# Kernel tuning notes

Hardware: AMD Instinct MI355X
Metric: run time of the kernel (lower is better)

Reference implementation:

```python
import jax, jax.numpy as jnp
import numpy as np

N_GRAPHS = 32
NUM_NODES = 2848
N = N_GRAPHS * NUM_NODES  # 91136
E = 1_000_000
K = 3   # num_stacks
T = 5   # num_layers
HID = 32
EPS = 1e-5


def setup_inputs() -> dict:
    key = jax.random.key(0)
    ks = jax.random.split(key, 32)
    s = 0.1
    rn = lambda k, shp: (jax.random.normal(k, shp, jnp.float32) * s)
    inp = {
        "x": jax.random.normal(ks[0], (N, 2), jnp.float32),
        "edge_index": jax.random.randint(ks[1], (2, E), 0, N, dtype=jnp.int32).astype(jnp.int64),
        "weights": jax.random.uniform(ks[2], (E,), jnp.float32),
        "batch": (jnp.arange(N) // NUM_NODES).astype(jnp.int64),
        # ARMAConv1: 2 -> 32
        "iw1": rn(ks[3], (K, 2, HID)),
        "w1": rn(ks[4], (T - 1, K, HID, HID)),
        "rw1": rn(ks[5], (T, K, 2, HID)),
        "b1": rn(ks[6], (T, K, 1, HID)),
        "g1": jnp.ones((HID,), jnp.float32), "be1": jnp.zeros((HID,), jnp.float32),
        # ARMAConv2: 32 -> 32
        "iw2": rn(ks[7], (K, HID, HID)),
        "w2": rn(ks[8], (T - 1, K, HID, HID)),
        "rw2": rn(ks[9], (T, K, HID, HID)),
        "b2": rn(ks[10], (T, K, 1, HID)),
        "g2": jnp.ones((HID,), jnp.float32), "be2": jnp.zeros((HID,), jnp.float32),
        # ARMAConv3: 32 -> 1
        "iw3": rn(ks[11], (K, HID, 1)),
        "w3": rn(ks[12], (T - 1, K, 1, 1)),
        "rw3": rn(ks[13], (T, K, HID, 1)),
        "b3": rn(ks[14], (T, K, 1, 1)),
        "g3": jnp.ones((1,), jnp.float32), "be3": jnp.zeros((1,), jnp.float32),
        # classifier Linear(1, 1)
        "cw": rn(ks[15], (1, 1)),
        "cb": jnp.zeros((1,), jnp.float32),
    }
    return inp


def gcn_norm(row, col, w, n):
    # deg over targets, sym normalization, no self loops (PyG ARMAConv default)
    deg = jnp.zeros((n,), w.dtype).at[col].add(w)
    dis = jnp.where(deg > 0, jax.lax.rsqrt(jnp.where(deg > 0, deg, 1.0)), 0.0)
    return dis[row] * w * dis[col]


def arma_conv(x, row, col, norm, iw, w, rw, b):
    # x: [N, Fin]; returns [N, Fout] (mean over K stacks)
    out = None
    for t in range(T):
        if t == 0:
            h = jnp.einsum('nf,kfo->kno', x, iw)          # [K, N, Fout]
        else:
            h = jnp.einsum('kno,kop->knp', out, w[t - 1])
        msg = h[:, row, :] * norm[None, :, None]           # [K, E, Fout]
        agg = jnp.zeros_like(h).at[:, col, :].add(msg)     # scatter to targets
        out = jax.nn.relu(agg + jnp.einsum('nf,kfo->kno', x, rw[t]) + b[t])
    return out.mean(axis=0)


def batch_norm(x, g, b):
    m = x.mean(axis=0)
    v = x.var(axis=0)  # biased, as torch BatchNorm1d (training stats)
    return (x - m) * jax.lax.rsqrt(v + EPS) * g + b


def reference(x, edge_index, weights, batch,
              iw1, w1, rw1, b1, g1, be1,
              iw2, w2, rw2, b2, g2, be2,
              iw3, w3, rw3, b3, g3, be3,
              cw, cb):
    row, col = edge_index[0], edge_index[1]
    norm = gcn_norm(row, col, weights, N)

    h = arma_conv(x, row, col, norm, iw1, w1, rw1, b1)
    h = jax.nn.relu(batch_norm(h, g1, be1))
    h = arma_conv(h, row, col, norm, iw2, w2, rw2, b2)
    h = jax.nn.relu(batch_norm(h, g2, be2))
    h = arma_conv(h, row, col, norm, iw3, w3, rw3, b3)
    h = jax.nn.relu(batch_norm(h, g3, be3))  # [N, 1]

    # to_dense_batch: each graph has exactly NUM_NODES nodes -> reshape
    xd = h.reshape(N_GRAPHS, NUM_NODES, 1)
    logits_nodes = (xd @ cw.T + cb).squeeze(-1)   # [B, NUM_NODES]
    logits_graph = logits_nodes.max(axis=1)       # [B]
    return logits_nodes, logits_graph
```

## Files before the change

kernel.cpp:

```cpp
#include <hip/hip_runtime.h>
#include <hip/hip_fp16.h>

#define N_GRAPHS 32
#define NUM_NODES 2848
#define NTOT (N_GRAPHS * NUM_NODES)
#define NE 1000000
#define KS 3
#define TL 5
#define HID 32
#define EPSV 1e-5f
#define SCAN_B 256
#define NBLK (NTOT / SCAN_B)
#define NBINS 64
#define CNTN (NBINS * NBLK)
#define CNTB (CNTN / SCAN_B)
#define NT8 (NTOT * 8)
#define NB128 (NTOT / 128)
#define SRCMASK 0x1FFFFu

typedef unsigned uintx4 __attribute__((ext_vector_type(4)));


__device__ __forceinline__ float2 unpk(unsigned u) {
    return make_float2(__uint_as_float(u << 16), __uint_as_float(u & 0xffff0000u));
}
__device__ __forceinline__ unsigned bf16rn(float f) {
    unsigned x = __float_as_uint(f);
    return (x + 0x7fffu + ((x >> 16) & 1u)) >> 16;
}
__device__ __forceinline__ unsigned pk(float a, float b) {
    return bf16rn(a) | (bf16rn(b) << 16);
}
__device__ __forceinline__ float dec_nm(unsigned q) {
    return __half2float(__ushort_as_half((unsigned short)(q >> 17)));
}


__global__ void k_cnt(const int* __restrict__ col, int* __restrict__ indegS) {
    int e = blockIdx.x * blockDim.x + threadIdx.x;
    if (e < NE) atomicAdd(&indegS[(col[e] << 2) | (e & 3)], 1);
}

__global__ void k_merge(const int* __restrict__ indegS, int* __restrict__ indeg) {
    int n = blockIdx.x * blockDim.x + threadIdx.x;
    if (n < NTOT) {
        int4 v = ((const int4*)indegS)[n];
        indeg[n] = v.x + v.y + v.z + v.w;
    }
}

__global__ void k_lhist(const int* __restrict__ indeg, int* __restrict__ cnt) {
    __shared__ int h[NBINS];
    int t = threadIdx.x;
    if (t < NBINS) h[t] = 0;
    __syncthreads();
    int n = blockIdx.x * SCAN_B + t;
    atomicAdd(&h[min(indeg[n], NBINS - 1)], 1);
    __syncthreads();
    if (t < NBINS) cnt[t * NBLK + blockIdx.x] = h[t];
}

__global__ void k_scan1(const int* __restrict__ in, int* __restrict__ bsum) {
    __shared__ int s[SCAN_B];
    int i = blockIdx.x * SCAN_B + threadIdx.x;
    s[threadIdx.x] = in[i];
    __syncthreads();
    for (int st = SCAN_B / 2; st >= 1; st >>= 1) {
        if (threadIdx.x < st) s[threadIdx.x] += s[threadIdx.x + st];
        __syncthreads();
    }
    if (threadIdx.x == 0) bsum[blockIdx.x] = s[0];
}

__global__ void k_scan2(int* __restrict__ bsum, int n) {
    __shared__ int s[512];
    int t = threadIdx.x;
    int v = (t < n) ? bsum[t] : 0;
    s[t] = v;
    __syncthreads();
    for (int off = 1; off < 512; off <<= 1) {
        int a = (t >= off) ? s[t - off] : 0;
        __syncthreads();
        s[t] += a;
        __syncthreads();
    }
    if (t < n) bsum[t] = s[t] - v;
}

__global__ void k_scan3(const int* __restrict__ in, const int* __restrict__ bsum,
                        int* __restrict__ out, int sentIdx, int sentVal) {
    __shared__ int s[SCAN_B];
    int i = blockIdx.x * SCAN_B + threadIdx.x;
    int v = in[i];
    s[threadIdx.x] = v;
    __syncthreads();
    for (int off = 1; off < SCAN_B; off <<= 1) {
        int a = (threadIdx.x >= off) ? s[threadIdx.x - off] : 0;
        __syncthreads();
        s[threadIdx.x] += a;
        __syncthreads();
    }
    out[i] = bsum[blockIdx.x] + s[threadIdx.x] - v;
    if (i == 0 && sentIdx >= 0) out[sentIdx] = sentVal;
}

__global__ void k_rank(const int* __restrict__ indeg, const int* __restrict__ cnt,
                       int* __restrict__ perm, int* __restrict__ invperm,
                       int* __restrict__ indegp) {
    __shared__ int base[NBINS];
    __shared__ int cur[NBINS];
    int t = threadIdx.x;
    if (t < NBINS) { base[t] = cnt[t * NBLK + blockIdx.x]; cur[t] = 0; }
    __syncthreads();
    int n = blockIdx.x * SCAN_B + t;
    int dg = indeg[n];
    int b = min(dg, NBINS - 1);
    int pos = base[b] + atomicAdd(&cur[b], 1);
    perm[pos] = n;
    invperm[n] = pos;
    indegp[pos] = dg;
}

__global__ void k_xp(const float2* __restrict__ x, const int* __restrict__ perm,
                     float2* __restrict__ xp) {
    int i = blockIdx.x * blockDim.x + threadIdx.x;
    if (i < NTOT) xp[i] = x[perm[i]];
}

__global__ void k_fill(const int* __restrict__ row, const int* __restrict__ col,
                       const float* __restrict__ w, const int* __restrict__ invperm,
                       int* __restrict__ cursor, unsigned* __restrict__ adjc) {
    int e = blockIdx.x * blockDim.x + threadIdx.x;
    if (e < NE) {
        int pr = invperm[row[e]], pc = invperm[col[e]];
        int p = atomicAdd(&cursor[pc], 1);
        unsigned short hb = __half_as_ushort(__float2half(w[e]));
        adjc[p] = ((unsigned)hb << 17) | (unsigned)pr;
    }
}

__global__ void k_degdis(const unsigned* __restrict__ adjc, const int* __restrict__ offs,
                         float* __restrict__ disp) {
    int n = blockIdx.x * blockDim.x + threadIdx.x;
    if (n >= NTOT) return;
    int e0 = offs[n], e1 = offs[n + 1];
    float d = 0.f;
    for (int e = e0; e < e1; ++e) d += dec_nm(adjc[e]);
    disp[n] = (d > 0.f) ? rsqrtf(d) : 0.f;
}

__global__ void k_norm(unsigned* __restrict__ adjc, const int* __restrict__ offs,
                       const float* __restrict__ disp) {
    int n = blockIdx.x * blockDim.x + threadIdx.x;
    if (n >= NTOT) return;
    float dc = disp[n];
    int e0 = offs[n], e1 = offs[n + 1];
    for (int e = e0; e < e1; ++e) {
        unsigned q = adjc[e];
        float nm = dc * dec_nm(q) * disp[q & SRCMASK];
        unsigned short hb = __half_as_ushort(__float2half(nm));
        adjc[e] = ((unsigned)hb << 17) | (q & SRCMASK);
    }
}


__global__ __launch_bounds__(256) void k_gath(
    const unsigned* __restrict__ SRC, const int* __restrict__ offs,
    const unsigned* __restrict__ adjc, unsigned* __restrict__ P) {
    int tid = threadIdx.x;
    int u = tid & 1;
    int nl = tid >> 1;
    int bid = blockIdx.x;
    int s = bid / NB128;
    int node = (bid - s * NB128) * 128 + nl;
    const uintx4* src = (const uintx4*)(SRC + (size_t)s * NT8);
    float a0 = 0.f, a1 = 0.f, a2 = 0.f, a3 = 0.f, a4 = 0.f, a5 = 0.f, a6 = 0.f, a7 = 0.f;
    int e0 = offs[node], e1 = offs[node + 1];
    int e = e0;
    for (; e + 4 <= e1; e += 4) {
        unsigned q0 = __builtin_nontemporal_load(adjc + e);
        unsigned q1 = __builtin_nontemporal_load(adjc + e + 1);
        unsigned q2 = __builtin_nontemporal_load(adjc + e + 2);
        unsigned q3 = __builtin_nontemporal_load(adjc + e + 3);
        uintx4 v0 = src[(q0 & SRCMASK) * 2 + u];
        uintx4 v1 = src[(q1 & SRCMASK) * 2 + u];
        uintx4 v2 = src[(q2 & SRCMASK) * 2 + u];
        uintx4 v3 = src[(q3 & SRCMASK) * 2 + u];
        float n0 = dec_nm(q0), n1 = dec_nm(q1), n2 = dec_nm(q2), n3 = dec_nm(q3);
        float2 t;
        t = unpk(v0.x); a0 += n0 * t.x; a1 += n0 * t.y;
        t = unpk(v0.y); a2 += n0 * t.x; a3 += n0 * t.y;
        t = unpk(v0.z); a4 += n0 * t.x; a5 += n0 * t.y;
        t = unpk(v0.w); a6 += n0 * t.x; a7 += n0 * t.y;
        t = unpk(v1.x); a0 += n1 * t.x; a1 += n1 * t.y;
        t = unpk(v1.y); a2 += n1 * t.x; a3 += n1 * t.y;
        t = unpk(v1.z); a4 += n1 * t.x; a5 += n1 * t.y;
        t = unpk(v1.w); a6 += n1 * t.x; a7 += n1 * t.y;
        t = unpk(v2.x); a0 += n2 * t.x; a1 += n2 * t.y;
        t = unpk(v2.y); a2 += n2 * t.x; a3 += n2 * t.y;
        t = unpk(v2.z); a4 += n2 * t.x; a5 += n2 * t.y;
        t = unpk(v2.w); a6 += n2 * t.x; a7 += n2 * t.y;
        t = unpk(v3.x); a0 += n3 * t.x; a1 += n3 * t.y;
        t = unpk(v3.y); a2 += n3 * t.x; a3 += n3 * t.y;
        t = unpk(v3.z); a4 += n3 * t.x; a5 += n3 * t.y;
        t = unpk(v3.w); a6 += n3 * t.x; a7 += n3 * t.y;
    }
    for (; e < e1; ++e) {
        unsigned q0 = __builtin_nontemporal_load(adjc + e);
        uintx4 v0 = src[(q0 & SRCMASK) * 2 + u];
        float n0 = dec_nm(q0);
        float2 t;
        t = unpk(v0.x); a0 += n0 * t.x; a1 += n0 * t.y;
        t = unpk(v0.y); a2 += n0 * t.x; a3 += n0 * t.y;
        t = unpk(v0.z); a4 += n0 * t.x; a5 += n0 * t.y;
        t = unpk(v0.w); a6 += n0 * t.x; a7 += n0 * t.y;
    }
    uintx4 o;
    o.x = pk(a0, a1); o.y = pk(a2, a3); o.z = pk(a4, a5); o.w = pk(a6, a7);
    __builtin_nontemporal_store(o, (uintx4*)(P + (size_t)s * NT8 + (size_t)node * 8) + u);
}


template<int FIN, bool PERK, bool LAST>
__global__ __launch_bounds__(256) void k_xform(
    const unsigned* __restrict__ P, const float* __restrict__ xin,
    const float* __restrict__ W, const float* __restrict__ rw,
    const float* __restrict__ bb, unsigned* __restrict__ OUTn,
    float* __restrict__ xm, float* __restrict__ stats) {
    constexpr int NSEC = PERK ? 6 : 2;
    constexpr int ND = 128;
    __shared__ unsigned sp[KS][ND][17];
    __shared__ float xr[FIN == 32 ? ND : 1][FIN == 32 ? 33 : 1];
    int tid = threadIdx.x;
    int node0 = blockIdx.x * ND;
    for (int t4 = tid; t4 < NSEC * 256; t4 += 256) {
        int s = t4 >> 8, r = t4 & 255, n = r >> 1, u4 = (r & 1) * 4;
        uintx4 v = *(const uintx4*)(P + (size_t)s * NT8 + (size_t)(node0 + n) * 8 + u4);
        int kk = PERK ? (s >> 1) : 0;
        int base = (s & 1) * 8 + u4;
        sp[kk][n][base]     = v.x;
        sp[kk][n][base + 1] = v.y;
        sp[kk][n][base + 2] = v.z;
        sp[kk][n][base + 3] = v.w;
    }
    if constexpr (FIN == 32) {
        for (int t4 = tid; t4 < ND * 8; t4 += 256) {
            int n = t4 >> 3, j4 = (t4 & 7) * 4;
            float4 v = ((const float4*)xin)[(size_t)(node0 + n) * 8 + (t4 & 7)];
            xr[n][j4] = v.x; xr[n][j4 + 1] = v.y; xr[n][j4 + 2] = v.z; xr[n][j4 + 3] = v.w;
        }
    }
    __syncthreads();
    int f2 = tid & 15, nl = tid >> 4;
    int nbase = nl * 8;
    float2 xv2[8];
    if constexpr (FIN == 2) {
#pragma unroll
        for (int n = 0; n < 8; ++n) xv2[n] = ((const float2*)xin)[node0 + nbase + n];
    }
    float m0[8] = {}, m1[8] = {};
    unsigned uo[KS][8];
#pragma unroll
    for (int k = 0; k < KS; ++k) {
        const int kk = PERK ? k : 0;
        float2 bv = ((const float2*)(bb + k * HID))[f2];
        float h0[8], h1[8];
#pragma unroll
        for (int n = 0; n < 8; ++n) { h0[n] = bv.x; h1[n] = bv.y; }
        const float2* W2 = (const float2*)(W + (size_t)k * HID * HID);
        const float2* R2 = (const float2*)(rw + (size_t)k * FIN * HID);
#pragma unroll 4
        for (int i2 = 0; i2 < 16; ++i2) {
            float2 wf0 = W2[(2 * i2) * 16 + f2];
            float2 wf1 = W2[(2 * i2 + 1) * 16 + f2];
            float2 rf0, rf1;
            if constexpr (FIN == 32) {
                rf0 = R2[(2 * i2) * 16 + f2];
                rf1 = R2[(2 * i2 + 1) * 16 + f2];
            }
#pragma unroll
            for (int n = 0; n < 8; ++n) {
                float2 sv = unpk(sp[kk][nbase + n][i2]);
                h0[n] += sv.x * wf0.x + sv.y * wf1.x;
                h1[n] += sv.x * wf0.y + sv.y * wf1.y;
                if constexpr (FIN == 32) {
                    float x0 = xr[nbase + n][2 * i2], x1 = xr[nbase + n][2 * i2 + 1];
                    h0[n] += x0 * rf0.x + x1 * rf1.x;
                    h1[n] += x0 * rf0.y + x1 * rf1.y;
                }
            }
        }
        if constexpr (FIN == 2) {
            float2 r0 = R2[0 * 16 + f2], r1 = R2[1 * 16 + f2];
#pragma unroll
            for (int n = 0; n < 8; ++n) {
                h0[n] += xv2[n].x * r0.x + xv2[n].y * r1.x;
                h1[n] += xv2[n].x * r0.y + xv2[n].y * r1.y;
            }
        }
#pragma unroll
        for (int n = 0; n < 8; ++n) {
            h0[n] = fmaxf(h0[n], 0.f);
            h1[n] = fmaxf(h1[n], 0.f);
            if constexpr (LAST) {
                m0[n] += h0[n]; m1[n] += h1[n];
            } else {
                uo[k][n] = pk(h0[n], h1[n]);
            }
        }
    }
    if constexpr (LAST) {
        float sv0 = 0.f, sq0 = 0.f, sv1 = 0.f, sq1 = 0.f;
#pragma unroll
        for (int n = 0; n < 8; ++n) {
            float v0 = m0[n] * (1.f / 3.f), v1 = m1[n] * (1.f / 3.f);
            ((float2*)xm)[(size_t)(node0 + nbase + n) * 16 + f2] = make_float2(v0, v1);
            sv0 += v0; sq0 += v0 * v0;
            sv1 += v1; sq1 += v1 * v1;
        }
        float* red = (float*)sp;
        __syncthreads();
        red[0 * 256 + f2 * 16 + nl] = sv0;
        red[1 * 256 + f2 * 16 + nl] = sq0;
        red[2 * 256 + f2 * 16 + nl] = sv1;
        red[3 * 256 + f2 * 16 + nl] = sq1;
        __syncthreads();
        if (nl == 0) {
            float a = 0.f, b = 0.f, c = 0.f, d = 0.f;
#pragma unroll
            for (int j = 0; j < 16; ++j) {
                a += red[0 * 256 + f2 * 16 + j];
                b += red[1 * 256 + f2 * 16 + j];
                c += red[2 * 256 + f2 * 16 + j];
                d += red[3 * 256 + f2 * 16 + j];
            }
            atomicAdd(&stats[2 * f2], a);
            atomicAdd(&stats[HID + 2 * f2], b);
            atomicAdd(&stats[2 * f2 + 1], c);
            atomicAdd(&stats[HID + 2 * f2 + 1], d);
        }
    } else {
#pragma unroll
        for (int k = 0; k < KS; ++k)
#pragma unroll
            for (int n = 0; n < 8; ++n)
                sp[k][nbase + n][f2] = uo[k][n];
        __syncthreads();
        for (int t4 = tid; t4 < 6 * 256; t4 += 256) {
            int s = t4 >> 8, r = t4 & 255, n = r >> 1, u4 = (r & 1) * 4;
            int kk = s >> 1;
            int base = (s & 1) * 8 + u4;
            uintx4 v;
            v.x = sp[kk][n][base];
            v.y = sp[kk][n][base + 1];
            v.z = sp[kk][n][base + 2];
            v.w = sp[kk][n][base + 3];
            __builtin_nontemporal_store(
                v, (uintx4*)(OUTn + (size_t)s * NT8 + (size_t)(node0 + n) * 8 + u4));
        }
    }
}


__global__ void k_gath2(const float2* __restrict__ xp, const int* __restrict__ offs,
                        const unsigned* __restrict__ adjc, float2* __restrict__ pag) {
    int node = blockIdx.x * blockDim.x + threadIdx.x;
    if (node >= NTOT) return;
    float a0 = 0.f, a1 = 0.f;
    int e0 = offs[node], e1 = offs[node + 1];
    int e = e0;
    for (; e + 4 <= e1; e += 4) {
        unsigned q0 = __builtin_nontemporal_load(adjc + e);
        unsigned q1 = __builtin_nontemporal_load(adjc + e + 1);
        unsigned q2 = __builtin_nontemporal_load(adjc + e + 2);
        unsigned q3 = __builtin_nontemporal_load(adjc + e + 3);
        float2 x0 = xp[q0 & SRCMASK], x1 = xp[q1 & SRCMASK];
        float2 x2 = xp[q2 & SRCMASK], x3 = xp[q3 & SRCMASK];
        float n0 = dec_nm(q0), n1 = dec_nm(q1), n2 = dec_nm(q2), n3 = dec_nm(q3);
        a0 += n0 * x0.x + n1 * x1.x + n2 * x2.x + n3 * x3.x;
        a1 += n0 * x0.y + n1 * x1.y + n2 * x2.y + n3 * x3.y;
    }
    for (; e < e1; ++e) {
        unsigned q0 = __builtin_nontemporal_load(adjc + e);
        float2 xs = xp[q0 & SRCMASK];
        float nm = dec_nm(q0);
        a0 += nm * xs.x; a1 += nm * xs.y;
    }
    pag[node] = make_float2(a0, a1);
}

__global__ void k_x0(const float2* __restrict__ pag, const float2* __restrict__ xp,
                     const float* __restrict__ iw, const float* __restrict__ rw0,
                     const float* __restrict__ b0, unsigned* __restrict__ OUT) {
    int tid = blockIdx.x * blockDim.x + threadIdx.x;
    int f2 = tid & 15;
    int node = tid >> 4;
    float2 pv = pag[node];
    float2 xn = xp[node];
#pragma unroll
    for (int k = 0; k < KS; ++k) {
        const float2* iw2 = (const float2*)(iw + k * 2 * HID);
        const float2* rw2 = (const float2*)(rw0 + k * 2 * HID);
        float2 wi0 = iw2[0 * 16 + f2], wi1 = iw2[1 * 16 + f2];
        float2 wr0 = rw2[0 * 16 + f2], wr1 = rw2[1 * 16 + f2];
        float2 bv = ((const float2*)(b0 + k * HID))[f2];
        float o0 = fmaxf(pv.x * wi0.x + pv.y * wi1.x + xn.x * wr0.x + xn.y * wr1.x + bv.x, 0.f);
        float o1 = fmaxf(pv.x * wi0.y + pv.y * wi1.y + xn.x * wr0.y + xn.y * wr1.y + bv.y, 0.f);
        OUT[(size_t)(k * 2 + (f2 >> 3)) * NT8 + (size_t)node * 8 + (f2 & 7)] = pk(o0, o1);
    }
}


__global__ void k_rec3(const float* __restrict__ xb, const float* __restrict__ iw3,
                       const float* __restrict__ rw3, const float* __restrict__ b3,
                       float4* __restrict__ H0, float4* __restrict__ RT) {
    int n = blockIdx.x * blockDim.x + threadIdx.x;
    if (n >= NTOT) return;
    float xr[HID];
#pragma unroll
    for (int j = 0; j < 8; ++j) {
        float4 v = ((const float4*)xb)[(size_t)n * 8 + j];
        xr[4 * j] = v.x; xr[4 * j + 1] = v.y; xr[4 * j + 2] = v.z; xr[4 * j + 3] = v.w;
    }
    {
        float a0 = 0.f, a1 = 0.f, a2 = 0.f;
#pragma unroll
        for (int i = 0; i < HID; ++i) {
            a0 += xr[i] * iw3[0 * HID + i];
            a1 += xr[i] * iw3[1 * HID + i];
            a2 += xr[i] * iw3[2 * HID + i];
        }
        H0[n] = make_float4(a0, a1, a2, 0.f);
    }
#pragma unroll
    for (int t = 0; t < TL; ++t) {
        float a0 = b3[t * KS + 0], a1 = b3[t * KS + 1], a2 = b3[t * KS + 2];
        const float* r = rw3 + (size_t)t * KS * HID;
#pragma unroll
        for (int i = 0; i < HID; ++i) {
            a0 += xr[i] * r[0 * HID + i];
            a1 += xr[i] * r[1 * HID + i];
            a2 += xr[i] * r[2 * HID + i];
        }
        RT[(size_t)t * NTOT + n] = make_float4(a0, a1, a2, 0.f);
    }
}

template<bool LAST>
__global__ void k_prop1(const float4* __restrict__ H, const float4* __restrict__ RT,
                        const float* __restrict__ W_t, const int* __restrict__ offs,
                        const unsigned* __restrict__ adjc, const int* __restrict__ perm,
                        float* __restrict__ outp) {
    int node = blockIdx.x * blockDim.x + threadIdx.x;
    if (node >= NTOT) return;
    float4 rt = RT[node];
    float a0 = rt.x, a1 = rt.y, a2 = rt.z;
    int e0 = offs[node], e1 = offs[node + 1];
    int e = e0;
    for (; e + 4 <= e1; e += 4) {
        unsigned q0 = __builtin_nontemporal_load(adjc + e);
        unsigned q1 = __builtin_nontemporal_load(adjc + e + 1);
        unsigned q2 = __builtin_nontemporal_load(adjc + e + 2);
        unsigned q3 = __builtin_nontemporal_load(adjc + e + 3);
        float4 h0 = H[q0 & SRCMASK], h1 = H[q1 & SRCMASK];
        float4 h2 = H[q2 & SRCMASK], h3 = H[q3 & SRCMASK];
        float n0 = dec_nm(q0), n1 = dec_nm(q1), n2 = dec_nm(q2), n3 = dec_nm(q3);
        a0 += n0 * h0.x; a1 += n0 * h0.y; a2 += n0 * h0.z;
        a0 += n1 * h1.x; a1 += n1 * h1.y; a2 += n1 * h1.z;
        a0 += n2 * h2.x; a1 += n2 * h2.y; a2 += n2 * h2.z;
        a0 += n3 * h3.x; a1 += n3 * h3.y; a2 += n3 * h3.z;
    }
    for (; e < e1; ++e) {
        unsigned q0 = __builtin_nontemporal_load(adjc + e);
        float4 h = H[q0 & SRCMASK];
        float nm = dec_nm(q0);
        a0 += nm * h.x; a1 += nm * h.y; a2 += nm * h.z;
    }
    a0 = fmaxf(a0, 0.f); a1 = fmaxf(a1, 0.f); a2 = fmaxf(a2, 0.f);
    if constexpr (LAST) {
        outp[perm[node]] = (a0 + a1 + a2) * (1.f / 3.f);
    } else {
        ((float4*)outp)[node] = make_float4(a0 * W_t[0], a1 * W_t[1], a2 * W_t[2], 0.f);
    }
}


__global__ void k_bnstats(const float* __restrict__ x, float* __restrict__ stats, int F) {
    __shared__ float s1[256];
    __shared__ float s2[256];
    int tid = threadIdx.x;
    int gid = blockIdx.x * blockDim.x + tid;
    int stride = gridDim.x * blockDim.x;
    int total = NTOT * F;
    float a = 0.f, b = 0.f;
    for (int i = gid; i < total; i += stride) {
        float v = x[i];
        a += v;
        b += v * v;
    }
    s1[tid] = a; s2[tid] = b;
    __syncthreads();
    for (int s = 128; s >= F; s >>= 1) {
        if (tid < s) { s1[tid] += s1[tid + s]; s2[tid] += s2[tid + s]; }
        __syncthreads();
    }
    if (tid < F) {
        atomicAdd(&stats[tid], s1[tid]);
        atomicAdd(&stats[F + tid], s2[tid]);
    }
}

__global__ void k_bnapply32(float* __restrict__ x, const float* __restrict__ stats,
                            const float* __restrict__ g, const float* __restrict__ be,
                            unsigned* __restrict__ xbf) {
    int tid = blockIdx.x * blockDim.x + threadIdx.x;
    int f2 = tid & 15;
    int node = tid >> 4;
    int f0 = 2 * f2, f1 = f0 + 1;
    float mm0 = stats[f0] * (1.f / NTOT);
    float vv0 = stats[HID + f0] * (1.f / NTOT) - mm0 * mm0;
    float mm1 = stats[f1] * (1.f / NTOT);
    float vv1 = stats[HID + f1] * (1.f / NTOT) - mm1 * mm1;
    float y0 = fmaxf((x[(size_t)node * 32 + f0] - mm0) * rsqrtf(vv0 + EPSV) * g[f0] + be[f0], 0.f);
    float y1 = fmaxf((x[(size_t)node * 32 + f1] - mm1) * rsqrtf(vv1 + EPSV) * g[f1] + be[f1], 0.f);
    x[(size_t)node * 32 + f0] = y0;
    x[(size_t)node * 32 + f1] = y1;
    if (xbf) xbf[(size_t)(f2 >> 3) * NT8 + (size_t)node * 8 + (f2 & 7)] = pk(y0, y1);
}

__global__ void k_bnapply1(float* __restrict__ x, const float* __restrict__ stats,
                           const float* __restrict__ g, const float* __restrict__ be) {
    int i = blockIdx.x * blockDim.x + threadIdx.x;
    if (i >= NTOT) return;
    float m = stats[0] * (1.f / NTOT);
    float v = stats[1] * (1.f / NTOT) - m * m;
    float y = (x[i] - m) * rsqrtf(v + EPSV) * g[0] + be[0];
    x[i] = fmaxf(y, 0.f);
}


__global__ void k_final(const float* __restrict__ h, const float* __restrict__ cw,
                        const float* __restrict__ cb, float* __restrict__ out) {
    __shared__ float smax[256];
    int g = blockIdx.x;
    float cwv = cw[0], cbv = cb[0];
    float mx = -INFINITY;
    for (int i = threadIdx.x; i < NUM_NODES; i += blockDim.x) {
        int nidx = g * NUM_NODES + i;
        float v = h[nidx] * cwv + cbv;
        out[nidx] = v;
        mx = fmaxf(mx, v);
    }
    smax[threadIdx.x] = mx;
    __syncthreads();
    for (int s = 128; s >= 1; s >>= 1) {
        if (threadIdx.x < s) smax[threadIdx.x] = fmaxf(smax[threadIdx.x], smax[threadIdx.x + s]);
        __syncthreads();
    }
    if (threadIdx.x == 0) out[NTOT + g] = smax[0];
}


extern "C" void kernel_launch(void* const* d_in, const int* in_sizes, int n_in,
                              void* d_out, int out_size, void* d_ws, size_t ws_size,
                              hipStream_t stream) {
    const float* x   = (const float*)d_in[0];
    const int*   ei  = (const int*)d_in[1];
    const int*   row = ei;
    const int*   col = ei + NE;
    const float* wts = (const float*)d_in[2];
    const float* iw1 = (const float*)d_in[4];
    const float* w1  = (const float*)d_in[5];
    const float* rw1 = (const float*)d_in[6];
    const float* b1  = (const float*)d_in[7];
    const float* g1  = (const float*)d_in[8];
    const float* be1 = (const float*)d_in[9];
    const float* iw2 = (const float*)d_in[10];
    const float* w2  = (const float*)d_in[11];
    const float* rw2 = (const float*)d_in[12];
    const float* b2  = (const float*)d_in[13];
    const float* g2  = (const float*)d_in[14];
    const float* be2 = (const float*)d_in[15];
    const float* iw3 = (const float*)d_in[16];
    const float* w3  = (const float*)d_in[17];
    const float* rw3 = (const float*)d_in[18];
    const float* b3  = (const float*)d_in[19];
    const float* g3  = (const float*)d_in[20];
    const float* be3 = (const float*)d_in[21];
    const float* cw  = (const float*)d_in[22];
    const float* cb  = (const float*)d_in[23];
    float* out = (float*)d_out;

    char* p = (char*)d_ws;
    auto alloc = [&](size_t bytes) {
        char* r = p;
        p += (bytes + 255) & ~(size_t)255;
        return r;
    };
    int*      indegS = (int*)alloc((size_t)NTOT * 16);
    int*      cnt    = (int*)alloc((size_t)CNTN * 4);
    float*    stats  = (float*)alloc(3 * 2 * HID * 4);
    char*     zend   = p;
    int*      indeg  = (int*)alloc((size_t)NTOT * 4);
    int*      bsum   = (int*)alloc((size_t)NBLK * 4);
    int*      offs   = (int*)alloc((size_t)(NTOT + 1) * 4);
    int*      cursor = (int*)alloc((size_t)NTOT * 4);
    int*      perm   = (int*)alloc((size_t)NTOT * 4);
    int*      invperm= (int*)alloc((size_t)NTOT * 4);
    int*      indegp = (int*)alloc((size_t)NTOT * 4);
    float*    disp   = (float*)alloc((size_t)NTOT * 4);
    unsigned* adjc   = (unsigned*)alloc((size_t)NE * 4);
    unsigned* OUTA   = (unsigned*)alloc((size_t)6 * NT8 * 4);
    unsigned* OUTB   = (unsigned*)alloc((size_t)6 * NT8 * 4);
    unsigned* P      = (unsigned*)alloc((size_t)6 * NT8 * 4);
    unsigned* xplane = (unsigned*)alloc((size_t)2 * NT8 * 4);
    float2*   xp     = (float2*)alloc((size_t)NTOT * 8);
    float2*   pag    = (float2*)alloc((size_t)NTOT * 8);
    float*    xa     = (float*)alloc((size_t)NTOT * HID * 4);
    float*    xb     = (float*)alloc((size_t)NTOT * HID * 4);
    float*    xc     = (float*)alloc((size_t)NTOT * 4);
    float4*   RT     = (float4*)alloc((size_t)TL * NTOT * 16);
    if ((size_t)(p - (char*)d_ws) > ws_size) return;

    const int tb = 256;
    const int ebl = (NE + tb - 1) / tb;
    const int nbl = NTOT / tb;
    const int g16 = NTOT * 16 / tb;

    hipMemsetAsync(indegS, 0, (size_t)(zend - (char*)indegS), stream);

    k_cnt<<<ebl, tb, 0, stream>>>(col, indegS);
    k_merge<<<nbl, tb, 0, stream>>>(indegS, indeg);
    k_lhist<<<NBLK, SCAN_B, 0, stream>>>(indeg, cnt);
    k_scan1<<<CNTB, SCAN_B, 0, stream>>>(cnt, bsum);
    k_scan2<<<1, 512, 0, stream>>>(bsum, CNTB);
    k_scan3<<<CNTB, SCAN_B, 0, stream>>>(cnt, bsum, cnt, -1, 0);
    k_rank<<<NBLK, SCAN_B, 0, stream>>>(indeg, cnt, perm, invperm, indegp);
    k_xp<<<nbl, tb, 0, stream>>>((const float2*)x, perm, xp);
    k_scan1<<<NBLK, SCAN_B, 0, stream>>>(indegp, bsum);
    k_scan2<<<1, 512, 0, stream>>>(bsum, NBLK);
    k_scan3<<<NBLK, SCAN_B, 0, stream>>>(indegp, bsum, offs, NTOT, NE);
    hipMemcpyAsync(cursor, offs, (size_t)NTOT * 4, hipMemcpyDeviceToDevice, stream);
    k_fill<<<ebl, tb, 0, stream>>>(row, col, wts, invperm, cursor, adjc);
    k_degdis<<<nbl, tb, 0, stream>>>(adjc, offs, disp);
    k_norm<<<nbl, tb, 0, stream>>>(adjc, offs, disp);

    {
        k_gath2<<<nbl, tb, 0, stream>>>(xp, offs, adjc, pag);
        k_x0<<<g16, tb, 0, stream>>>(pag, xp, iw1, rw1, b1, OUTA);
        unsigned* Hc = OUTA; unsigned* Hn = OUTB;
        for (int t = 1; t < TL - 1; ++t) {
            k_gath<<<6 * NB128, tb, 0, stream>>>(Hc, offs, adjc, P);
            k_xform<2, true, false><<<NB128, tb, 0, stream>>>(
                P, (const float*)xp, w1 + (size_t)(t - 1) * KS * HID * HID,
                rw1 + (size_t)t * KS * 2 * HID, b1 + (size_t)t * KS * HID, Hn,
                nullptr, nullptr);
            unsigned* tmp = Hc; Hc = Hn; Hn = tmp;
        }
        k_gath<<<6 * NB128, tb, 0, stream>>>(Hc, offs, adjc, P);
        k_xform<2, true, true><<<NB128, tb, 0, stream>>>(
            P, (const float*)xp, w1 + (size_t)(TL - 2) * KS * HID * HID,
            rw1 + (size_t)(TL - 1) * KS * 2 * HID, b1 + (size_t)(TL - 1) * KS * HID,
            nullptr, xa, stats);
        k_bnapply32<<<g16, tb, 0, stream>>>(xa, stats, g1, be1, xplane);
    }
    {
        k_gath<<<2 * NB128, tb, 0, stream>>>(xplane, offs, adjc, P);
        k_xform<32, false, false><<<NB128, tb, 0, stream>>>(
            P, xa, iw2, rw2, b2, OUTA, nullptr, nullptr);
        unsigned* Hc = OUTA; unsigned* Hn = OUTB;
        for (int t = 1; t < TL - 1; ++t) {
            k_gath<<<6 * NB128, tb, 0, stream>>>(Hc, offs, adjc, P);
            k_xform<32, true, false><<<NB128, tb, 0, stream>>>(
                P, xa, w2 + (size_t)(t - 1) * KS * HID * HID,
                rw2 + (size_t)t * KS * HID * HID, b2 + (size_t)t * KS * HID, Hn,
                nullptr, nullptr);
            unsigned* tmp = Hc; Hc = Hn; Hn = tmp;
        }
        k_gath<<<6 * NB128, tb, 0, stream>>>(Hc, offs, adjc, P);
        k_xform<32, true, true><<<NB128, tb, 0, stream>>>(
            P, xa, w2 + (size_t)(TL - 2) * KS * HID * HID,
            rw2 + (size_t)(TL - 1) * KS * HID * HID, b2 + (size_t)(TL - 1) * KS * HID,
            nullptr, xb, stats + 2 * HID);
        k_bnapply32<<<g16, tb, 0, stream>>>(xb, stats + 2 * HID, g2, be2, nullptr);
    }
    {
        float4* HAf = (float4*)OUTA;
        float4* HBf = (float4*)OUTB;
        k_rec3<<<nbl, tb, 0, stream>>>(xb, iw3, rw3, b3, HAf, RT);
        const float4* Hc = HAf; float4* Hn = HBf;
        for (int t = 0; t < TL - 1; ++t) {
            k_prop1<false><<<nbl, tb, 0, stream>>>(
                Hc, RT + (size_t)t * NTOT, w3 + (size_t)t * KS, offs, adjc, perm, (float*)Hn);
            const float4* tmp = Hc; Hc = Hn; Hn = (float4*)tmp;
        }
        k_prop1<true><<<nbl, tb, 0, stream>>>(
            Hc, RT + (size_t)(TL - 1) * NTOT, nullptr, offs, adjc, perm, xc);
        k_bnstats<<<256, tb, 0, stream>>>(xc, stats + 4 * HID, 1);
        k_bnapply1<<<nbl, tb, 0, stream>>>(xc, stats + 4 * HID, g3, be3);
    }

    k_final<<<N_GRAPHS, 256, 0, stream>>>(xc, cw, cb, out);
}
```

Measured before the change: 1.177 ms.

## Stream per-stack inputs through shared memory and store xin as packed bf16

The transform kernel no longer stages all three stacks' propagated features at once. It loads one stack slice per iteration into a single shared buffer and writes each stack's output right after computing it, which shrinks LDS use and removes the uo[KS][8] register array. The FIN=32 input rows are now kept in shared memory as packed bf16 pairs instead of fp32, which also lowers precision on that term. The aim is higher occupancy from less LDS and fewer registers, at the cost of extra __syncthreads per stack and less memory-level parallelism within each block.

```diff
diff --git a/kernel.cpp b/kernel.cpp
--- a/kernel.cpp
+++ b/kernel.cpp
@@ -227,30 +227,31 @@
     const float* __restrict__ W, const float* __restrict__ rw,
     const float* __restrict__ bb, unsigned* __restrict__ OUTn,
     float* __restrict__ xm, float* __restrict__ stats) {
-    constexpr int NSEC = PERK ? 6 : 2;
     constexpr int ND = 128;
-    __shared__ unsigned sp[KS][ND][17];
-    __shared__ float xr[FIN == 32 ? ND : 1][FIN == 32 ? 33 : 1];
+    __shared__ unsigned spi[ND][17];
+    __shared__ unsigned spo[LAST ? 1 : ND][LAST ? 1 : 17];
+    __shared__ unsigned xr[FIN == 32 ? ND : 1][FIN == 32 ? 17 : 1];
     int tid = threadIdx.x;
     int node0 = blockIdx.x * ND;
-    for (int t4 = tid; t4 < NSEC * 256; t4 += 256) {
-        int s = t4 >> 8, r = t4 & 255, n = r >> 1, u4 = (r & 1) * 4;
-        uintx4 v = *(const uintx4*)(P + (size_t)s * NT8 + (size_t)(node0 + n) * 8 + u4);
-        int kk = PERK ? (s >> 1) : 0;
-        int base = (s & 1) * 8 + u4;
-        sp[kk][n][base]     = v.x;
-        sp[kk][n][base + 1] = v.y;
-        sp[kk][n][base + 2] = v.z;
-        sp[kk][n][base + 3] = v.w;
-    }
+
     if constexpr (FIN == 32) {
         for (int t4 = tid; t4 < ND * 8; t4 += 256) {
-            int n = t4 >> 3, j4 = (t4 & 7) * 4;
-            float4 v = ((const float4*)xin)[(size_t)(node0 + n) * 8 + (t4 & 7)];
-            xr[n][j4] = v.x; xr[n][j4 + 1] = v.y; xr[n][j4 + 2] = v.z; xr[n][j4 + 3] = v.w;
-        }
-    }
-    __syncthreads();
+            int n = t4 >> 3, j = t4 & 7;
+            float4 v = ((const float4*)xin)[(size_t)(node0 + n) * 8 + j];
+            xr[n][2 * j]     = pk(v.x, v.y);
+            xr[n][2 * j + 1] = pk(v.z, v.w);
+        }
+    }
+    if constexpr (!PERK) {
+        for (int t4 = tid; t4 < 2 * 256; t4 += 256) {
+            int s2 = t4 >> 8, r = t4 & 255, n = r >> 1, u4 = (r & 1) * 4;
+            uintx4 v = *(const uintx4*)(P + (size_t)s2 * NT8 + (size_t)(node0 + n) * 8 + u4);
+            int base = s2 * 8 + u4;
+            spi[n][base] = v.x; spi[n][base + 1] = v.y;
+            spi[n][base + 2] = v.z; spi[n][base + 3] = v.w;
+        }
+    }
+
     int f2 = tid & 15, nl = tid >> 4;
     int nbase = nl * 8;
     float2 xv2[8];
@@ -259,10 +260,22 @@
         for (int n = 0; n < 8; ++n) xv2[n] = ((const float2*)xin)[node0 + nbase + n];
     }
     float m0[8] = {}, m1[8] = {};
-    unsigned uo[KS][8];
+
 #pragma unroll
     for (int k = 0; k < KS; ++k) {
-        const int kk = PERK ? k : 0;
+        __syncthreads();
+        if constexpr (PERK) {
+            for (int t4 = tid; t4 < 2 * 256; t4 += 256) {
+                int s2 = t4 >> 8, r = t4 & 255, n = r >> 1, u4 = (r & 1) * 4;
+                int s = k * 2 + s2;
+                uintx4 v = *(const uintx4*)(P + (size_t)s * NT8 + (size_t)(node0 + n) * 8 + u4);
+                int base = s2 * 8 + u4;
+                spi[n][base] = v.x; spi[n][base + 1] = v.y;
+                spi[n][base + 2] = v.z; spi[n][base + 3] = v.w;
+            }
+        }
+        __syncthreads();
+
         float2 bv = ((const float2*)(bb + k * HID))[f2];
         float h0[8], h1[8];
 #pragma unroll
@@ -280,13 +293,13 @@
             }
 #pragma unroll
             for (int n = 0; n < 8; ++n) {
-                float2 sv = unpk(sp[kk][nbase + n][i2]);
+                float2 sv = unpk(spi[nbase + n][i2]);
                 h0[n] += sv.x * wf0.x + sv.y * wf1.x;
                 h1[n] += sv.x * wf0.y + sv.y * wf1.y;
                 if constexpr (FIN == 32) {
-                    float x0 = xr[nbase + n][2 * i2], x1 = xr[nbase + n][2 * i2 + 1];
-                    h0[n] += x0 * rf0.x + x1 * rf1.x;
-                    h1[n] += x0 * rf0.y + x1 * rf1.y;
+                    float2 xq = unpk(xr[nbase + n][i2]);
+                    h0[n] += xq.x * rf0.x + xq.y * rf1.x;
+                    h1[n] += xq.x * rf0.y + xq.y * rf1.y;
                 }
             }
         }
@@ -298,17 +311,31 @@
                 h1[n] += xv2[n].x * r0.y + xv2[n].y * r1.y;
             }
         }
-#pragma unroll
-        for (int n = 0; n < 8; ++n) {
-            h0[n] = fmaxf(h0[n], 0.f);
-            h1[n] = fmaxf(h1[n], 0.f);
-            if constexpr (LAST) {
-                m0[n] += h0[n]; m1[n] += h1[n];
-            } else {
-                uo[k][n] = pk(h0[n], h1[n]);
+
+        if constexpr (LAST) {
+#pragma unroll
+            for (int n = 0; n < 8; ++n) {
+                m0[n] += fmaxf(h0[n], 0.f);
+                m1[n] += fmaxf(h1[n], 0.f);
             }
-        }
-    }
+        } else {
+#pragma unroll
+            for (int n = 0; n < 8; ++n)
+                spo[nbase + n][f2] = pk(fmaxf(h0[n], 0.f), fmaxf(h1[n], 0.f));
+            __syncthreads();
+            for (int t4 = tid; t4 < 2 * 256; t4 += 256) {
+                int s2 = t4 >> 8, r = t4 & 255, n = r >> 1, u4 = (r & 1) * 4;
+                int so = k * 2 + s2;
+                int base = s2 * 8 + u4;
+                uintx4 v;
+                v.x = spo[n][base]; v.y = spo[n][base + 1];
+                v.z = spo[n][base + 2]; v.w = spo[n][base + 3];
+                __builtin_nontemporal_store(
+                    v, (uintx4*)(OUTn + (size_t)so * NT8 + (size_t)(node0 + n) * 8 + u4));
+            }
+        }
+    }
+
     if constexpr (LAST) {
         float sv0 = 0.f, sq0 = 0.f, sv1 = 0.f, sq1 = 0.f;
 #pragma unroll
@@ -318,7 +345,7 @@
             sv0 += v0; sq0 += v0 * v0;
             sv1 += v1; sq1 += v1 * v1;
         }
-        float* red = (float*)sp;
+        float* red = (float*)spi;
         __syncthreads();
         red[0 * 256 + f2 * 16 + nl] = sv0;
         red[1 * 256 + f2 * 16 + nl] = sq0;
@@ -338,25 +365,6 @@
             atomicAdd(&stats[HID + 2 * f2], b);
             atomicAdd(&stats[2 * f2 + 1], c);
             atomicAdd(&stats[HID + 2 * f2 + 1], d);
-        }
-    } else {
-#pragma unroll
-        for (int k = 0; k < KS; ++k)
-#pragma unroll
-            for (int n = 0; n < 8; ++n)
-                sp[k][nbase + n][f2] = uo[k][n];
-        __syncthreads();
-        for (int t4 = tid; t4 < 6 * 256; t4 += 256) {
-            int s = t4 >> 8, r = t4 & 255, n = r >> 1, u4 = (r & 1) * 4;
-            int kk = s >> 1;
-            int base = (s & 1) * 8 + u4;
-            uintx4 v;
-            v.x = sp[kk][n][base];
-            v.y = sp[kk][n][base + 1];
-            v.z = sp[kk][n][base + 2];
-            v.w = sp[kk][n][base + 3];
-            __builtin_nontemporal_store(
-                v, (uintx4*)(OUTn + (size_t)s * NT8 + (size_t)(node0 + n) * 8 + u4));
         }
     }
 }
```

After: 1.190 ms. Within noise of the previous version (+1.1%).
